# Performance work log

Hardware: AMD Instinct MI355X
Metric: run time of the kernel (lower is better)

Reference implementation:

```python
import jax, jax.numpy as jnp
import numpy as np

T = 4      # num_step (also LSTM num_layers)
R = 64     # num_relation (= LSTM hidden size)
E = 1024   # num_entity
B = 128    # batch
IN = R + 2 * E  # LSTM input size


def _lstm_layer(x_seq, Wih, Whh, bih, bhh):
    # x_seq: [T, B, In]; torch gate order i, f, g, o
    Bsz = x_seq.shape[1]
    H = Whh.shape[1]
    pre = jnp.einsum('tbi,gi->tbg', x_seq, Wih) + bih + bhh  # [T,B,4H]

    def step(carry, z):
        h, c = carry
        z = z + h @ Whh.T
        i, f, g, o = jnp.split(z, 4, axis=-1)
        i, f, o = jax.nn.sigmoid(i), jax.nn.sigmoid(f), jax.nn.sigmoid(o)
        c = f * c + i * jnp.tanh(g)
        h = o * jnp.tanh(c)
        return (h, c), h

    init = (jnp.zeros((Bsz, H), x_seq.dtype), jnp.zeros((Bsz, H), x_seq.dtype))
    _, hs = jax.lax.scan(step, init, pre)
    return hs  # [T, B, H]


def setup_inputs() -> dict:
    key = jax.random.key(0)
    ks = jax.random.split(key, 12)
    s = 0.05
    inp = {
        'x': jax.random.uniform(ks[0], (B, IN), dtype=jnp.float32),
        'kb': jax.random.uniform(ks[1], (R, E, E), dtype=jnp.float32) * 0.01,
        # LSTM layer 0 (input dim IN)
        'Wih0': jax.random.normal(ks[2], (4 * R, IN), dtype=jnp.float32) * s,
        'Whh0': jax.random.normal(ks[3], (4 * R, R), dtype=jnp.float32) * s,
        'bih0': jnp.zeros((4 * R,), jnp.float32),
        'bhh0': jnp.zeros((4 * R,), jnp.float32),
        # LSTM layers 1..T-1 (input dim R)
        'Wih': jax.random.normal(ks[4], (T - 1, 4 * R, R), dtype=jnp.float32) * s,
        'Whh': jax.random.normal(ks[5], (T - 1, 4 * R, R), dtype=jnp.float32) * s,
        'bih': jnp.zeros((T - 1, 4 * R), jnp.float32),
        'bhh': jnp.zeros((T - 1, 4 * R), jnp.float32),
    }
    return inp


def reference(x, kb, Wih0, Whh0, bih0, bhh0, Wih, Whh, bih, bhh):
    # input to LSTM: x repeated T times -> [T, B, IN]
    seq = jnp.broadcast_to(x[None], (T,) + x.shape)
    hs = _lstm_layer(seq, Wih0, Whh0, bih0, bhh0)
    for l in range(T - 1):  # small fixed layer count
        hs = _lstm_layer(hs, Wih[l], Whh[l], bih[l], bhh[l])
    h = jax.nn.softmax(hs, axis=-1)  # [T, B, R] (first softmax)

    mem = [x[:, R:R + E]]  # memory[0] = head entity vector, [B, E]
    for i in range(T):
        h2 = jax.nn.softmax(h[i], axis=-1)  # double softmax, faithful to source
        # causal memory attention over steps k <= i
        att = jax.nn.softmax(jnp.einsum('kbr,br->bk', h[:i + 1], h[i]), axis=-1)  # [B, i+1]
        prev = jnp.einsum('bk,kbe->be', att, jnp.stack(mem))  # [B, E]
        # per-relation operator application: sum_r h2[b,r] * KB[r] @ prev[b]
        tmp = jnp.einsum('ref,bf->bre', kb, prev)  # [B, R, E]
        mem.append(jnp.einsum('br,bre->be', h2, tmp))

    tail = x[:, R + E:R + 2 * E]  # [B, E]
    score = jax.nn.sigmoid(-jnp.einsum('be,be->b', mem[-1], tail))[:, None]  # [B, 1]
    return score
```

## Files before the change

### kernel.cpp

```cpp
#include <hip/hip_runtime.h>
#include <cstdint>
#include <cstddef>

#define B_ 128
#define E_ 1024
#define R_ 64
#define T_ 4
#define IN_ 2112
#define G_ 256

typedef __attribute__((ext_vector_type(4))) float f32x4;
typedef __attribute__((ext_vector_type(8))) __bf16 bf16x8;

#define KB_SCALE 64.0f
#define KB_INV_SCALE (1.0f / 64.0f)

__device__ __forceinline__ unsigned short f2bf(float f) {
  unsigned int u = __float_as_uint(f);
  u += 0x7fffu + ((u >> 16) & 1u);
  return (unsigned short)(u >> 16);
}
__device__ __forceinline__ float bf2f(unsigned short u) {
  return __uint_as_float(((unsigned int)u) << 16);
}
__device__ __forceinline__ unsigned int pack2(float lo, float hi) {
  return (unsigned int)f2bf(lo) | ((unsigned int)f2bf(hi) << 16);
}
__device__ __forceinline__ unsigned char f2fp8(float v) {
  int r = __builtin_amdgcn_cvt_pk_fp8_f32(v, 0.f, 0, false);
  return (unsigned char)(r & 0xff);
}
__device__ __forceinline__ float wred_sum(float v) {
#pragma unroll
  for (int m = 32; m > 0; m >>= 1) v += __shfl_xor(v, m, 64);
  return v;
}
__device__ __forceinline__ float wred_max(float v) {
#pragma unroll
  for (int m = 32; m > 0; m >>= 1) v = fmaxf(v, __shfl_xor(v, m, 64));
  return v;
}
__device__ __forceinline__ float sigmoidf_(float x) { return 1.f / (1.f + expf(-x)); }

__device__ __forceinline__ void gload_lds16(const void* g, void* l) {
  __builtin_amdgcn_global_load_lds(
      (const __attribute__((address_space(1))) unsigned int*)g,
      (__attribute__((address_space(3))) unsigned int*)l, 16, 0, 0);
}

__global__ __launch_bounds__(256) void conv_kernel(
    const float* __restrict__ kb, unsigned char* __restrict__ kbf8) {
  const size_t base = (size_t)blockIdx.x * 8192 + (size_t)threadIdx.x * 32;
  int w[8];
#pragma unroll
  for (int j = 0; j < 8; j++) {
    float4 v = *(const float4*)(kb + base + j * 4);
    int r = __builtin_amdgcn_cvt_pk_fp8_f32(v.x * KB_SCALE, v.y * KB_SCALE, 0, false);
    r = __builtin_amdgcn_cvt_pk_fp8_f32(v.z * KB_SCALE, v.w * KB_SCALE, r, true);
    w[j] = r;
  }
  uint4 u0 = {(unsigned)w[0], (unsigned)w[1], (unsigned)w[2], (unsigned)w[3]};
  uint4 u1 = {(unsigned)w[4], (unsigned)w[5], (unsigned)w[6], (unsigned)w[7]};
  *(uint4*)(kbf8 + base) = u0;
  *(uint4*)(kbf8 + base + 16) = u1;
}

__global__ __launch_bounds__(256) void recur_kernel(
    const float* __restrict__ x,
    const float* __restrict__ Wih0, const float* __restrict__ Whh0,
    const float* __restrict__ bih0, const float* __restrict__ bhh0,
    const float* __restrict__ Wih, const float* __restrict__ Whh,
    const float* __restrict__ bih, const float* __restrict__ bhh,
    float* __restrict__ h2_out, float* __restrict__ att_out,
    unsigned char* __restrict__ prevq) {
  __shared__ float Wt[G_ * 65];
  __shared__ float xrow[IN_];
  __shared__ float hbuf[R_], cbuf[R_], zbuf[G_];
  __shared__ float hs_in[T_][R_], hs_out[T_][R_], hmat[T_][R_];
  const int tid = threadIdx.x;
  const int b = blockIdx.x;
  const int lane = tid & 63, wv = tid >> 6;

  for (int l = tid; l < IN_; l += 256) xrow[l] = x[b * IN_ + l];
  __syncthreads();
  float p0 = bih0[tid] + bhh0[tid];
  {
    const float* wr = Wih0 + (size_t)tid * IN_;
#pragma unroll 4
    for (int j = 0; j < IN_; j += 4) {
      float4 w = *(const float4*)(wr + j);
      p0 += xrow[j] * w.x + xrow[j + 1] * w.y + xrow[j + 2] * w.z + xrow[j + 3] * w.w;
    }
  }
  {
    int w = __builtin_amdgcn_cvt_pk_fp8_f32(xrow[R_ + tid * 4], xrow[R_ + tid * 4 + 1], 0, false);
    w = __builtin_amdgcn_cvt_pk_fp8_f32(xrow[R_ + tid * 4 + 2], xrow[R_ + tid * 4 + 3], w, true);
    ((int*)prevq)[b * 256 + tid] = w;
  }

  auto stage_w = [&](const float* src) {
    for (int l = tid; l < G_ * 16; l += 256) {
      int g = l >> 4, c4 = (l & 15) * 4;
      const float4 v = *(const float4*)(src + g * R_ + c4);
      float* dst = &Wt[g * 65 + c4];
      dst[0] = v.x; dst[1] = v.y; dst[2] = v.z; dst[3] = v.w;
    }
  };
  auto scan = [&](float* pret) {
    for (int t = 0; t < T_; t++) {
      float z = pret[t];
#pragma unroll
      for (int j = 0; j < R_; j++) z += hbuf[j] * Wt[tid * 65 + j];
      zbuf[tid] = z;
      __syncthreads();
      if (tid < R_) {
        float iv = sigmoidf_(zbuf[tid]);
        float fv = sigmoidf_(zbuf[R_ + tid]);
        float gv = tanhf(zbuf[2 * R_ + tid]);
        float ov = sigmoidf_(zbuf[3 * R_ + tid]);
        float c = fv * cbuf[tid] + iv * gv;
        cbuf[tid] = c;
        float h = ov * tanhf(c);
        hbuf[tid] = h;
        hs_out[t][tid] = h;
      }
      __syncthreads();
    }
  };

  float pret[T_];
#pragma unroll
  for (int t = 0; t < T_; t++) pret[t] = p0;
  stage_w(Whh0);
  if (tid < R_) { hbuf[tid] = 0.f; cbuf[tid] = 0.f; }
  __syncthreads();
  scan(pret);

  for (int l = 0; l < T_ - 1; l++) {
    hs_in[tid >> 6][tid & 63] = hs_out[tid >> 6][tid & 63];
    __syncthreads();
    stage_w(Wih + l * G_ * R_);
    __syncthreads();
    const float bsum = bih[l * G_ + tid] + bhh[l * G_ + tid];
    for (int t = 0; t < T_; t++) {
      float p = bsum;
#pragma unroll
      for (int j = 0; j < R_; j++) p += hs_in[t][j] * Wt[tid * 65 + j];
      pret[t] = p;
    }
    __syncthreads();
    stage_w(Whh + l * G_ * R_);
    if (tid < R_) { hbuf[tid] = 0.f; cbuf[tid] = 0.f; }
    __syncthreads();
    scan(pret);
  }

  {
    float v = hs_out[wv][lane];
    float mx = wred_max(v);
    float ev = expf(v - mx);
    float sm = wred_sum(ev);
    float hval = ev / sm;
    hmat[wv][lane] = hval;
    float mx2 = wred_max(hval);
    float e2 = expf(hval - mx2);
    float s2 = wred_sum(e2);
    h2_out[(wv * B_ + b) * R_ + lane] = e2 / s2;
    __syncthreads();
    float dots[T_];
    for (int k = 0; k <= wv; k++)
      dots[k] = wred_sum(hmat[k][lane] * hmat[wv][lane]);
    if (lane == 0) {
      float mx3 = dots[0];
      for (int k = 1; k <= wv; k++) mx3 = fmaxf(mx3, dots[k]);
      float ss = 0.f, es[T_];
      for (int k = 0; k <= wv; k++) { es[k] = expf(dots[k] - mx3); ss += es[k]; }
      for (int k = 0; k <= wv; k++) att_out[(wv * B_ + b) * 4 + k] = es[k] / ss;
    }
  }
}

__global__ __launch_bounds__(256) void gemm_f8_kernel(
    const unsigned char* __restrict__ Af8,
    const unsigned char* __restrict__ Kf8,
    unsigned short* __restrict__ part) {
  __shared__ unsigned char As[2][4096];
  __shared__ unsigned char Bs[2][4096];
  const int tid = threadIdx.x, wv = tid >> 6, lane = tid & 63;
  const int et = blockIdx.x, r = blockIdx.y;
  const int wm = (wv & 1) * 64, wn = (wv >> 1) * 64;
  const int fr = lane & 15, koff = (lane >> 4) * 8;

  const int srow = wv * 32 + (lane >> 1);
  const int shalf = (lane & 1) * 16;
  const unsigned char* agp = Af8 + (size_t)srow * 1024 + shalf;
  const unsigned char* bgp = Kf8 + (size_t)r * 1048576 + (size_t)(et * 128 + srow) * 1024 + shalf;

  f32x4 acc[4][4];
#pragma unroll
  for (int mt = 0; mt < 4; mt++)
#pragma unroll
    for (int nt = 0; nt < 4; nt++)
#pragma unroll
      for (int q = 0; q < 4; q++) acc[mt][nt][q] = 0.f;

  gload_lds16(agp, &As[0][wv * 1024]);
  gload_lds16(bgp, &Bs[0][wv * 1024]);

#pragma unroll 2
  for (int kk = 0; kk < 32; kk++) {
    const int cur = kk & 1;
    __syncthreads();
    if (kk < 31) {
      gload_lds16(agp + (kk + 1) * 32, &As[cur ^ 1][wv * 1024]);
      gload_lds16(bgp + (kk + 1) * 32, &Bs[cur ^ 1][wv * 1024]);
    }
    long af[4], bf[4];
#pragma unroll
    for (int mt = 0; mt < 4; mt++)
      af[mt] = *(const long*)(&As[cur][(wm + mt * 16 + fr) * 32 + koff]);
#pragma unroll
    for (int nt = 0; nt < 4; nt++)
      bf[nt] = *(const long*)(&Bs[cur][(wn + nt * 16 + fr) * 32 + koff]);
#pragma unroll
    for (int mt = 0; mt < 4; mt++)
#pragma unroll
      for (int nt = 0; nt < 4; nt++)
        acc[mt][nt] = __builtin_amdgcn_mfma_f32_16x16x32_fp8_fp8(af[mt], bf[nt], acc[mt][nt], 0, 0, 0);
  }
  const int crow = (lane >> 4) * 4;
  unsigned short* pout = part + (size_t)r * 131072;
#pragma unroll
  for (int mt = 0; mt < 4; mt++)
#pragma unroll
    for (int nt = 0; nt < 4; nt++)
#pragma unroll
      for (int q = 0; q < 4; q++)
        pout[(wm + mt * 16 + crow + q) * 1024 + et * 128 + wn + nt * 16 + fr] =
            f2bf(acc[mt][nt][q]);
}

__global__ __launch_bounds__(256) void mid_kernel(
    const unsigned short* __restrict__ part, const float* __restrict__ h2,
    const float* __restrict__ att, const float* __restrict__ x,
    float* __restrict__ mem, unsigned char* __restrict__ prevq, int it) {
  const int idx = blockIdx.x * 256 + threadIdx.x;
  const int b = idx >> 10, e = idx & 1023;
  const float* h2row = h2 + (it * B_ + b) * R_;
  const unsigned short* pp = part + idx;
  float s = 0.f;
#pragma unroll 8
  for (int rr = 0; rr < 64; rr++) s += h2row[rr] * bf2f(pp[(size_t)rr * 131072]);
  s *= KB_INV_SCALE;
  mem[it * 131072 + idx] = s;
  if (it < 3) {
    const float* arow = att + ((it + 1) * B_ + b) * 4;
    float acc = arow[0] * x[b * IN_ + R_ + e];
    for (int k = 1; k <= it; k++) acc += arow[k] * mem[(k - 1) * 131072 + idx];
    acc += arow[it + 1] * s;
    prevq[idx] = f2fp8(acc);
  }
}

__global__ __launch_bounds__(256) void prep_fp32_kernel(
    const float* __restrict__ x, const float* __restrict__ att,
    const float* __restrict__ mem, float* __restrict__ prev,
    float* __restrict__ newmem, int it) {
  const int idx = blockIdx.x * 256 + threadIdx.x;
  const int b = idx >> 10, e = idx & 1023;
  const float* arow = att + (it * B_ + b) * 4;
  float acc = arow[0] * x[b * IN_ + R_ + e];
  for (int k = 1; k <= it; k++)
    acc += arow[k] * mem[(k - 1) * (B_ * E_) + b * E_ + e];
  prev[idx] = acc;
  newmem[idx] = 0.f;
}

__global__ __launch_bounds__(256) void gemm_fp32_kernel(
    const float* __restrict__ prev, const float* __restrict__ h2,
    const float* __restrict__ kb, float* __restrict__ out) {
  __shared__ unsigned short As[128 * 40];
  __shared__ unsigned short Bs[128 * 40];
  __shared__ float h2s[128];
  const int tid = threadIdx.x;
  const int et = blockIdx.x;
  const int r = blockIdx.y;
  if (tid < 128) h2s[tid] = h2[tid * 64 + r];
  __syncthreads();
  const int row = tid >> 1;
  const int c0 = (tid & 1) * 16;
  const float hsc = h2s[row];
  const float* aptr = prev + row * 1024 + c0;
  const float* bptr = kb + (size_t)r * (1024u * 1024u) + (size_t)(et * 128 + row) * 1024 + c0;
  unsigned short* adst = As + row * 40 + c0;
  unsigned short* bdst = Bs + row * 40 + c0;
  const int wv = tid >> 6, lane = tid & 63;
  const int wm = (wv & 1) * 64, wn = (wv >> 1) * 64;
  const int fr = lane & 15, koff = (lane >> 4) * 8;
  f32x4 acc[4][4];
#pragma unroll
  for (int mt = 0; mt < 4; mt++)
#pragma unroll
    for (int nt = 0; nt < 4; nt++)
#pragma unroll
      for (int q = 0; q < 4; q++) acc[mt][nt][q] = 0.f;
  for (int kk = 0; kk < 32; kk++) {
    const float4 a0 = *(const float4*)(aptr + kk * 32);
    const float4 a1 = *(const float4*)(aptr + kk * 32 + 4);
    const float4 a2 = *(const float4*)(aptr + kk * 32 + 8);
    const float4 a3 = *(const float4*)(aptr + kk * 32 + 12);
    const float4 b0 = *(const float4*)(bptr + kk * 32);
    const float4 b1 = *(const float4*)(bptr + kk * 32 + 4);
    const float4 b2 = *(const float4*)(bptr + kk * 32 + 8);
    const float4 b3 = *(const float4*)(bptr + kk * 32 + 12);
    __syncthreads();
    uint4 u;
    u.x = pack2(a0.x * hsc, a0.y * hsc); u.y = pack2(a0.z * hsc, a0.w * hsc);
    u.z = pack2(a1.x * hsc, a1.y * hsc); u.w = pack2(a1.z * hsc, a1.w * hsc);
    *(uint4*)adst = u;
    u.x = pack2(a2.x * hsc, a2.y * hsc); u.y = pack2(a2.z * hsc, a2.w * hsc);
    u.z = pack2(a3.x * hsc, a3.y * hsc); u.w = pack2(a3.z * hsc, a3.w * hsc);
    *(uint4*)(adst + 8) = u;
    u.x = pack2(b0.x, b0.y); u.y = pack2(b0.z, b0.w);
    u.z = pack2(b1.x, b1.y); u.w = pack2(b1.z, b1.w);
    *(uint4*)bdst = u;
    u.x = pack2(b2.x, b2.y); u.y = pack2(b2.z, b2.w);
    u.z = pack2(b3.x, b3.y); u.w = pack2(b3.z, b3.w);
    *(uint4*)(bdst + 8) = u;
    __syncthreads();
    bf16x8 af[4], bfr[4];
#pragma unroll
    for (int mt = 0; mt < 4; mt++)
      af[mt] = *(const bf16x8*)(As + (wm + mt * 16 + fr) * 40 + koff);
#pragma unroll
    for (int nt = 0; nt < 4; nt++)
      bfr[nt] = *(const bf16x8*)(Bs + (wn + nt * 16 + fr) * 40 + koff);
#pragma unroll
    for (int mt = 0; mt < 4; mt++)
#pragma unroll
      for (int nt = 0; nt < 4; nt++)
        acc[mt][nt] = __builtin_amdgcn_mfma_f32_16x16x32_bf16(af[mt], bfr[nt], acc[mt][nt], 0, 0, 0);
  }
  const int crow = (lane >> 4) * 4;
  const int ccol = et * 128 + fr;
#pragma unroll
  for (int mt = 0; mt < 4; mt++)
#pragma unroll
    for (int nt = 0; nt < 4; nt++)
#pragma unroll
      for (int q = 0; q < 4; q++)
        atomicAdd(&out[(wm + mt * 16 + crow + q) * 1024 + ccol + wn + nt * 16], acc[mt][nt][q]);
}

__global__ __launch_bounds__(256) void score_kernel(
    const float* __restrict__ x, const float* __restrict__ mem4,
    float* __restrict__ out) {
  __shared__ float red[4];
  const int b = blockIdx.x, tid = threadIdx.x;
  float s = 0.f;
  for (int e = tid; e < E_; e += 256)
    s += mem4[b * E_ + e] * x[b * IN_ + R_ + E_ + e];
  s = wred_sum(s);
  if ((tid & 63) == 0) red[tid >> 6] = s;
  __syncthreads();
  if (tid == 0) {
    float t = red[0] + red[1] + red[2] + red[3];
    out[b] = 1.f / (1.f + expf(t));
  }
}

extern "C" void kernel_launch(void* const* d_in, const int* in_sizes, int n_in,
                              void* d_out, int out_size, void* d_ws, size_t ws_size,
                              hipStream_t stream) {
  const float* x    = (const float*)d_in[0];
  const float* kb   = (const float*)d_in[1];
  const float* Wih0 = (const float*)d_in[2];
  const float* Whh0 = (const float*)d_in[3];
  const float* bih0 = (const float*)d_in[4];
  const float* bhh0 = (const float*)d_in[5];
  const float* Wih  = (const float*)d_in[6];
  const float* Whh  = (const float*)d_in[7];
  const float* bih  = (const float*)d_in[8];
  const float* bhh  = (const float*)d_in[9];

  float* ws    = (float*)d_ws;
  float* h2    = ws;
  float* att   = ws + 32768;
  float* mem   = ws + 34816;
  float* prevq = ws + 559104;
  float* part  = ws + 690176;
  float* kbf8  = ws + 4884480;
  const size_t need_big = (size_t)(4884480 + 16777216) * sizeof(float);
  const bool big = ws_size >= need_big;

  if (big) {
    conv_kernel<<<8192, 256, 0, stream>>>(kb, (unsigned char*)kbf8);
    recur_kernel<<<128, 256, 0, stream>>>(x, Wih0, Whh0, bih0, bhh0,
                                          Wih, Whh, bih, bhh,
                                          h2, att, (unsigned char*)prevq);
    for (int i = 0; i < 4; i++) {
      gemm_f8_kernel<<<dim3(8, 64), 256, 0, stream>>>(
          (const unsigned char*)prevq, (const unsigned char*)kbf8,
          (unsigned short*)part);
      mid_kernel<<<512, 256, 0, stream>>>((const unsigned short*)part, h2, att, x,
                                          mem, (unsigned char*)prevq, i);
    }
  } else {
    recur_kernel<<<128, 256, 0, stream>>>(x, Wih0, Whh0, bih0, bhh0,
                                          Wih, Whh, bih, bhh,
                                          h2, att, (unsigned char*)prevq);
    for (int i = 0; i < 4; i++) {
      float* newmem = mem + i * (B_ * E_);
      prep_fp32_kernel<<<512, 256, 0, stream>>>(x, att, mem, prevq, newmem, i);
      gemm_fp32_kernel<<<dim3(8, 64), 256, 0, stream>>>(prevq, h2 + i * (B_ * R_), kb, newmem);
    }
  }
  score_kernel<<<128, 256, 0, stream>>>(x, mem + 3 * (B_ * E_), (float*)d_out);
}
```

Baseline: 654.5 us.

## Widen FP8 GEMM K-tile to 128 and drop double buffering

The FP8 MFMA GEMM now stages a 128-wide K slice of A and KB into shared memory per iteration, 8 iterations instead of 32. Each thread issues four 16-byte global-to-LDS loads per operand, and each K slice feeds four MFMA sub-steps between barriers. The ping-pong double buffer is removed, so each tile is loaded, waited on, computed, then fenced with a second barrier. This cuts barrier count and makes global loads longer and more coalesced, but loads no longer overlap compute and the 128-byte row stride may cause LDS bank conflicts.

```diff
diff --git a/kernel.cpp b/kernel.cpp
--- a/kernel.cpp
+++ b/kernel.cpp
@@ -184,17 +184,18 @@
     const unsigned char* __restrict__ Af8,
     const unsigned char* __restrict__ Kf8,
     unsigned short* __restrict__ part) {
-  __shared__ unsigned char As[2][4096];
-  __shared__ unsigned char Bs[2][4096];
+  __shared__ unsigned char As[128 * 128];
+  __shared__ unsigned char Bs[128 * 128];
   const int tid = threadIdx.x, wv = tid >> 6, lane = tid & 63;
   const int et = blockIdx.x, r = blockIdx.y;
   const int wm = (wv & 1) * 64, wn = (wv >> 1) * 64;
   const int fr = lane & 15, koff = (lane >> 4) * 8;
 
-  const int srow = wv * 32 + (lane >> 1);
-  const int shalf = (lane & 1) * 16;
-  const unsigned char* agp = Af8 + (size_t)srow * 1024 + shalf;
-  const unsigned char* bgp = Kf8 + (size_t)r * 1048576 + (size_t)(et * 128 + srow) * 1024 + shalf;
+  const int srow = wv * 32 + (lane >> 3);
+  const int scol = (lane & 7) * 16;
+  const unsigned char* agp = Af8 + (size_t)srow * 1024 + scol;
+  const unsigned char* bgp = Kf8 + (size_t)r * 1048576 +
+                             (size_t)(et * 128 + srow) * 1024 + scol;
 
   f32x4 acc[4][4];
 #pragma unroll
@@ -204,29 +205,30 @@
 #pragma unroll
       for (int q = 0; q < 4; q++) acc[mt][nt][q] = 0.f;
 
-  gload_lds16(agp, &As[0][wv * 1024]);
-  gload_lds16(bgp, &Bs[0][wv * 1024]);
-
-#pragma unroll 2
-  for (int kk = 0; kk < 32; kk++) {
-    const int cur = kk & 1;
-    __syncthreads();
-    if (kk < 31) {
-      gload_lds16(agp + (kk + 1) * 32, &As[cur ^ 1][wv * 1024]);
-      gload_lds16(bgp + (kk + 1) * 32, &Bs[cur ^ 1][wv * 1024]);
-    }
-    long af[4], bf[4];
-#pragma unroll
-    for (int mt = 0; mt < 4; mt++)
-      af[mt] = *(const long*)(&As[cur][(wm + mt * 16 + fr) * 32 + koff]);
-#pragma unroll
-    for (int nt = 0; nt < 4; nt++)
-      bf[nt] = *(const long*)(&Bs[cur][(wn + nt * 16 + fr) * 32 + koff]);
-#pragma unroll
-    for (int mt = 0; mt < 4; mt++)
+  for (int kk = 0; kk < 8; kk++) {
+#pragma unroll
+    for (int j = 0; j < 4; j++) {
+      gload_lds16(agp + kk * 128 + j * 8192, As + (wv * 32 + j * 8) * 128);
+      gload_lds16(bgp + kk * 128 + j * 8192, Bs + (wv * 32 + j * 8) * 128);
+    }
+    __syncthreads();
+#pragma unroll
+    for (int kc = 0; kc < 4; kc++) {
+      long af[4], bfr[4];
+#pragma unroll
+      for (int mt = 0; mt < 4; mt++)
+        af[mt] = *(const long*)(As + (wm + mt * 16 + fr) * 128 + kc * 32 + koff);
 #pragma unroll
       for (int nt = 0; nt < 4; nt++)
-        acc[mt][nt] = __builtin_amdgcn_mfma_f32_16x16x32_fp8_fp8(af[mt], bf[nt], acc[mt][nt], 0, 0, 0);
+        bfr[nt] = *(const long*)(Bs + (wn + nt * 16 + fr) * 128 + kc * 32 + koff);
+#pragma unroll
+      for (int mt = 0; mt < 4; mt++)
+#pragma unroll
+        for (int nt = 0; nt < 4; nt++)
+          acc[mt][nt] = __builtin_amdgcn_mfma_f32_16x16x32_fp8_fp8(
+              af[mt], bfr[nt], acc[mt][nt], 0, 0, 0);
+    }
+    __syncthreads();
   }
   const int crow = (lane >> 4) * 4;
   unsigned short* pout = part + (size_t)r * 131072;
```

After: 785.4 us. +20.0%, slower.
